# Kernel optimization log

Hardware: AMD Instinct MI355X
Metric: run time of the kernel (lower is better)

Reference implementation:

```python
import jax, jax.numpy as jnp
import numpy as np

N_STATE = 1024
N_HEAD = 16
B = 2
S = 2048


def setup_inputs() -> dict:
    key = jax.random.key(0)
    ks = jax.random.split(key, 8)
    s = 0.02
    x = jax.random.normal(ks[0], (B, S, N_STATE), dtype=jnp.float32)
    # causal additive mask, as in Whisper: upper triangle = -inf
    mask = jnp.where(jnp.triu(jnp.ones((S, S), dtype=bool), k=1), -jnp.inf, 0.0).astype(jnp.float32)
    Wq = jax.random.normal(ks[1], (N_STATE, N_STATE), dtype=jnp.float32) * s
    bq = jax.random.normal(ks[2], (N_STATE,), dtype=jnp.float32) * s
    Wk = jax.random.normal(ks[3], (N_STATE, N_STATE), dtype=jnp.float32) * s
    Wv = jax.random.normal(ks[4], (N_STATE, N_STATE), dtype=jnp.float32) * s
    bv = jax.random.normal(ks[5], (N_STATE,), dtype=jnp.float32) * s
    Wo = jax.random.normal(ks[6], (N_STATE, N_STATE), dtype=jnp.float32) * s
    bo = jax.random.normal(ks[7], (N_STATE,), dtype=jnp.float32) * s
    return {"x": x, "mask": mask, "Wq": Wq, "bq": bq, "Wk": Wk,
            "Wv": Wv, "bv": bv, "Wo": Wo, "bo": bo}


def reference(x, mask, Wq, bq, Wk, Wv, bv, Wo, bo):
    Bb, S_, D = x.shape
    H = N_HEAD
    hd = D // H
    scale = hd ** (-0.25)  # scale split across q and k, as in the source
    q = x @ Wq.T + bq              # [B,S,D]
    k = x @ Wk.T                   # key has no bias
    v = x @ Wv.T + bv
    # [B,S,D] -> [B,H,S,hd]
    q = q.reshape(Bb, S_, H, hd).transpose(0, 2, 1, 3) * scale
    k = k.reshape(Bb, S_, H, hd).transpose(0, 2, 1, 3) * scale
    v = v.reshape(Bb, S_, H, hd).transpose(0, 2, 1, 3)
    qk = jnp.einsum('bhsd,bhtd->bhst', q, k) + mask[:S_, :S_]
    w = jax.nn.softmax(qk, axis=-1).astype(q.dtype)
    out = jnp.einsum('bhst,bhtd->bhsd', w, v)
    out = out.transpose(0, 2, 1, 3).reshape(Bb, S_, D)
    return out @ Wo.T + bo
```

## Files before the change

kernel.cpp:

```cpp
#include <hip/hip_runtime.h>
#include <hip/hip_bf16.h>
#include <cmath>

typedef __bf16 bf16;
typedef __bf16 bf16x8 __attribute__((ext_vector_type(8)));
typedef __bf16 bf16x4 __attribute__((ext_vector_type(4)));
typedef float f32x4 __attribute__((ext_vector_type(4)));

#define QS 0.18033688f

__device__ __forceinline__ void load16_to_lds(const void* g, void* l) {
    __builtin_amdgcn_global_load_lds(
        (const __attribute__((address_space(1))) unsigned int*)g,
        (__attribute__((address_space(3))) unsigned int*)l, 16, 0, 0);
}

__global__ __launch_bounds__(256) void convert_kernel(
    const float* __restrict__ x,  const float* __restrict__ wq,
    const float* __restrict__ wk, const float* __restrict__ wv,
    const float* __restrict__ wo, bf16* __restrict__ dst)
{
    const size_t M1 = 1024ull * 1024ull, M4 = 4ull * M1;
    size_t i0 = ((size_t)blockIdx.x * 256 + threadIdx.x) * 8;
    const float* s;
    size_t off;
    float sc = 1.f;
    if      (i0 < M4)        { s = x;  off = i0; }
    else if (i0 < M4 + M1)   { s = wq; off = i0 - M4; sc = QS; }
    else if (i0 < M4 + 2*M1) { s = wk; off = i0 - M4 - M1; }
    else if (i0 < M4 + 3*M1) { s = wv; off = i0 - M4 - 2*M1; }
    else                     { s = wo; off = i0 - M4 - 3*M1; }
    float4 a = *(const float4*)(s + off);
    float4 b = *(const float4*)(s + off + 4);
    bf16x8 r = { (bf16)(a.x*sc), (bf16)(a.y*sc), (bf16)(a.z*sc), (bf16)(a.w*sc),
                 (bf16)(b.x*sc), (bf16)(b.y*sc), (bf16)(b.z*sc), (bf16)(b.w*sc) };
    *(bf16x8*)(dst + i0) = r;
}

template<int BM, bool OUT_F32>
__device__ __forceinline__ void gemm_core(
    const bf16* __restrict__ A, const bf16* __restrict__ W,
    const float* __restrict__ bias, void* __restrict__ C,
    int mb, int nb, bool vt_out, float bias_scale)
{
    constexpr int IF = BM / 32;
    __shared__ __align__(16) bf16 As[BM * 32];
    __shared__ __align__(16) bf16 Bs[128 * 32];

    const int tid  = threadIdx.x;
    const int lane = tid & 63;
    const int wave = tid >> 6;
    const int wr   = (wave >> 1) * (BM / 2);
    const int wc   = (wave & 1) * 64;
    const int l15  = lane & 15;
    const int l4   = lane >> 4;
    const int swz  = (l4 ^ ((l15 >> 1) & 3)) * 8;

    f32x4 acc[IF][4] = {};

    for (int kt = 0; kt < 32; ++kt) {
#pragma unroll
        for (int it = 0; it < BM / 64; ++it) {
            int c = it * 256 + tid;
            int scol = ((c & 3) ^ ((c >> 3) & 3)) * 8;
            load16_to_lds(&A[(size_t)(mb * BM + (c >> 2)) * 1024 + kt * 32 + scol],
                          &As[(it * 256 + (tid & 192)) * 8]);
        }
#pragma unroll
        for (int it = 0; it < 2; ++it) {
            int c = it * 256 + tid;
            int scol = ((c & 3) ^ ((c >> 3) & 3)) * 8;
            load16_to_lds(&W[(size_t)(nb * 128 + (c >> 2)) * 1024 + kt * 32 + scol],
                          &Bs[(it * 256 + (tid & 192)) * 8]);
        }
        __syncthreads();
        bf16x8 af[IF], bfr[4];
#pragma unroll
        for (int i = 0; i < IF; ++i)
            af[i] = *(const bf16x8*)&As[(wr + i * 16 + l15) * 32 + swz];
#pragma unroll
        for (int j = 0; j < 4; ++j)
            bfr[j] = *(const bf16x8*)&Bs[(wc + j * 16 + l15) * 32 + swz];
#pragma unroll
        for (int i = 0; i < IF; ++i)
#pragma unroll
            for (int j = 0; j < 4; ++j)
                acc[i][j] = __builtin_amdgcn_mfma_f32_16x16x32_bf16(
                    af[i], bfr[j], acc[i][j], 0, 0, 0);
        __syncthreads();
    }

    if (!OUT_F32 && vt_out) {
#pragma unroll
        for (int j = 0; j < 4; ++j) {
            int col = nb * 128 + wc + j * 16 + l15;
            float bv = bias ? bias[col] : 0.f;
            int h = col >> 6, d = col & 63;
#pragma unroll
            for (int i = 0; i < IF; ++i) {
                int m0 = mb * BM + wr + i * 16 + l4 * 4;
                int b = m0 >> 11, s = m0 & 2047;
                bf16x4 pk = { (bf16)(acc[i][j][0] + bv), (bf16)(acc[i][j][1] + bv),
                              (bf16)(acc[i][j][2] + bv), (bf16)(acc[i][j][3] + bv) };
                *(bf16x4*)&((bf16*)C)[(size_t)((b * 16 + h) * 64 + d) * 2048 + s] = pk;
            }
        }
    } else {
#pragma unroll
        for (int j = 0; j < 4; ++j) {
            int col = nb * 128 + wc + j * 16 + l15;
            float bv = bias ? bias[col] * bias_scale : 0.f;
#pragma unroll
            for (int i = 0; i < IF; ++i) {
                int row0 = mb * BM + wr + i * 16 + l4 * 4;
#pragma unroll
                for (int r = 0; r < 4; ++r) {
                    float val = acc[i][j][r] + bv;
                    size_t idx = (size_t)(row0 + r) * 1024 + col;
                    if (OUT_F32) ((float*)C)[idx] = val;
                    else         ((bf16*)C)[idx]  = (bf16)val;
                }
            }
        }
    }
}

__global__ __launch_bounds__(256) void qkv_kernel(
    const bf16* __restrict__ xb,
    const bf16* __restrict__ wqb, const float* __restrict__ bq,
    const bf16* __restrict__ wkb,
    const bf16* __restrict__ wvb, const float* __restrict__ bv,
    bf16* __restrict__ q, bf16* __restrict__ k, bf16* __restrict__ vt)
{
    int mb = blockIdx.x;
    int nbg = blockIdx.y;
    int sel = nbg >> 3, nb = nbg & 7;
    const bf16* W = (sel == 0) ? wqb : ((sel == 1) ? wkb : wvb);
    const float* bias = (sel == 0) ? bq : ((sel == 2) ? bv : nullptr);
    bf16* C = (sel == 0) ? q : ((sel == 1) ? k : vt);
    gemm_core<128, false>(xb, W, bias, C, mb, nb, sel == 2,
                          sel == 0 ? QS : 1.f);
}

__global__ __launch_bounds__(256) void oproj_kernel(
    const bf16* __restrict__ ao, const bf16* __restrict__ wob,
    const float* __restrict__ bo, float* __restrict__ out)
{
    gemm_core<128, true>(ao, wob, bo, out, blockIdx.x, blockIdx.y, false, 1.f);
}

__global__ __launch_bounds__(128) void attn_kernel(
    const bf16* __restrict__ q, const bf16* __restrict__ k,
    const bf16* __restrict__ vt, bf16* __restrict__ o)
{
    __shared__ __align__(16) bf16 Ks[2][64 * 64];
    __shared__ __align__(16) bf16 Vs[2][64 * 64];
    __shared__ __align__(16) bf16 Ps[2][32 * 72];

    const int tid  = threadIdx.x;
    const int lane = tid & 63;
    const int wave = tid >> 6;
    const int l15  = lane & 15;
    const int l4   = lane >> 4;

    const int bh = blockIdx.x;
    const int qt = 31 - blockIdx.y;
    const int b = bh >> 4, h = bh & 15;

    auto stage = [&](int nt, int buf) {
#pragma unroll
        for (int it = 0; it < 4; ++it) {
            int c = it * 128 + tid;
            int scol = ((c & 7) ^ ((c >> 3) & 7)) * 8;
            load16_to_lds(&k[(size_t)(b * 2048 + nt * 64 + (c >> 3)) * 1024 + h * 64 + scol],
                          &Ks[buf][(it * 128 + (tid & 64)) * 8]);
            load16_to_lds(&vt[(size_t)(bh * 64 + (c >> 3)) * 2048 + nt * 64 + scol],
                          &Vs[buf][(it * 128 + (tid & 64)) * 8]);
        }
    };

    int b0 = 0;
    stage(0, 0);

    const int qrow0 = qt * 64 + wave * 32;
    bf16x8 qf[2][2];
#pragma unroll
    for (int qb = 0; qb < 2; ++qb)
#pragma unroll
        for (int kk = 0; kk < 2; ++kk)
            qf[qb][kk] = *(const bf16x8*)&q[(size_t)(b * 2048 + qrow0 + qb * 16 + l15) * 1024
                                           + h * 64 + kk * 32 + l4 * 8];

    f32x4 oacc[2][4] = {};
    float lsum[2] = { 0.f, 0.f };

    const int n = qt + 1;
    for (int nt = 0; nt < n; ++nt) {
        __syncthreads();
        if (nt + 1 < n) stage(nt + 1, b0 ^ 1);

        f32x4 s[2][4] = {};
#pragma unroll
        for (int kk = 0; kk < 2; ++kk) {
#pragma unroll
            for (int j = 0; j < 4; ++j) {
                bf16x8 kf = *(const bf16x8*)&Ks[b0][(j * 16 + l15) * 64
                                + (((kk * 4 + l4) ^ (l15 & 7)) * 8)];
                s[0][j] = __builtin_amdgcn_mfma_f32_16x16x32_bf16(kf, qf[0][kk], s[0][j], 0, 0, 0);
                s[1][j] = __builtin_amdgcn_mfma_f32_16x16x32_bf16(kf, qf[1][kk], s[1][j], 0, 0, 0);
            }
        }

        const bool diag = (nt == qt);
#pragma unroll
        for (int qb = 0; qb < 2; ++qb) {
            float pv[4][4];
            if (diag) {
                int qg = qrow0 + qb * 16 + l15;
#pragma unroll
                for (int j = 0; j < 4; ++j)
#pragma unroll
                    for (int r = 0; r < 4; ++r) {
                        int kg = nt * 64 + j * 16 + l4 * 4 + r;
                        pv[j][r] = (kg > qg) ? 0.f : __builtin_amdgcn_exp2f(s[qb][j][r]);
                    }
            } else {
#pragma unroll
                for (int j = 0; j < 4; ++j)
#pragma unroll
                    for (int r = 0; r < 4; ++r)
                        pv[j][r] = __builtin_amdgcn_exp2f(s[qb][j][r]);
            }
#pragma unroll
            for (int j = 0; j < 4; ++j)
                lsum[qb] += (pv[j][0] + pv[j][1]) + (pv[j][2] + pv[j][3]);

#pragma unroll
            for (int j = 0; j < 4; ++j) {
                bf16x4 pk = { (bf16)pv[j][0], (bf16)pv[j][1], (bf16)pv[j][2], (bf16)pv[j][3] };
                *(bf16x4*)&Ps[wave][(qb * 16 + l15) * 72 + j * 16 + l4 * 4] = pk;
            }
        }

#pragma unroll
        for (int kk = 0; kk < 2; ++kk) {
            bf16x8 pf0 = *(const bf16x8*)&Ps[wave][l15 * 72 + kk * 32 + l4 * 8];
            bf16x8 pf1 = *(const bf16x8*)&Ps[wave][(16 + l15) * 72 + kk * 32 + l4 * 8];
#pragma unroll
            for (int f = 0; f < 4; ++f) {
                bf16x8 vf = *(const bf16x8*)&Vs[b0][(f * 16 + l15) * 64
                                + (((kk * 4 + l4) ^ (l15 & 7)) * 8)];
                oacc[0][f] = __builtin_amdgcn_mfma_f32_16x16x32_bf16(pf0, vf, oacc[0][f], 0, 0, 0);
                oacc[1][f] = __builtin_amdgcn_mfma_f32_16x16x32_bf16(pf1, vf, oacc[1][f], 0, 0, 0);
            }
        }
        b0 ^= 1;
    }

#pragma unroll
    for (int qb = 0; qb < 2; ++qb) {
        float ls = lsum[qb];
        ls += __shfl_xor(ls, 16, 64);
        ls += __shfl_xor(ls, 32, 64);
        float rinv[4];
#pragma unroll
        for (int r = 0; r < 4; ++r) rinv[r] = 1.f / __shfl(ls, l4 * 4 + r, 64);
#pragma unroll
        for (int f = 0; f < 4; ++f)
#pragma unroll
            for (int r = 0; r < 4; ++r)
                o[(size_t)(b * 2048 + qrow0 + qb * 16 + l4 * 4 + r) * 1024 + h * 64 + f * 16 + l15]
                    = (bf16)(oacc[qb][f][r] * rinv[r]);
    }
}

extern "C" void kernel_launch(void* const* d_in, const int* in_sizes, int n_in,
                              void* d_out, int out_size, void* d_ws, size_t ws_size,
                              hipStream_t stream)
{
    const float* x  = (const float*)d_in[0];
    const float* Wq = (const float*)d_in[2];
    const float* bq = (const float*)d_in[3];
    const float* Wk = (const float*)d_in[4];
    const float* Wv = (const float*)d_in[5];
    const float* bv = (const float*)d_in[6];
    const float* Wo = (const float*)d_in[7];
    const float* bo = (const float*)d_in[8];
    float* out = (float*)d_out;

    const size_t M1 = 1024ull * 1024ull, M4 = 4ull * M1;
    bf16* base = (bf16*)d_ws;
    bf16* xb  = base;
    bf16* wqb = base + M4;
    bf16* wkb = base + M4 + M1;
    bf16* wvb = base + M4 + 2 * M1;
    bf16* wob = base + M4 + 3 * M1;
    bf16* q   = base + 8 * M1;
    bf16* k   = base + 12 * M1;
    bf16* vt  = base + 16 * M1;
    bf16* ao  = xb;

    convert_kernel<<<4096, 256, 0, stream>>>(x, Wq, Wk, Wv, Wo, base);
    qkv_kernel<<<dim3(32, 24), 256, 0, stream>>>(xb, wqb, bq, wkb, wvb, bv, q, k, vt);
    attn_kernel<<<dim3(32, 32), 128, 0, stream>>>(q, k, vt, ao);
    oproj_kernel<<<dim3(32, 8), 256, 0, stream>>>(ao, wob, bo, out);
}
```

Before: 193.3 us.

## Write K/V in MFMA fragment order and read them directly from global in attention

The QKV GEMM epilogue now scatters K and V into a per-(batch,head,key-tile) layout that matches the MFMA operand fragments, so each lane reads one contiguous 16-byte chunk. The attention kernel drops its LDS double-buffered K/V staging and syncthreads, instead loading fragments straight from global/L2. It also uses one wave per 32-query block, with a grid twice as large and a launch bound of 4. This removes LDS staging and barriers, but the epilogue now does scalar scattered bf16 stores, and K/V tiles are re-read from cache by more waves.

```diff
diff --git a/kernel.cpp b/kernel.cpp
--- a/kernel.cpp
+++ b/kernel.cpp
@@ -37,11 +37,11 @@
     *(bf16x8*)(dst + i0) = r;
 }
 
-template<int BM, bool OUT_F32>
+template<int BM, int MODE>
 __device__ __forceinline__ void gemm_core(
     const bf16* __restrict__ A, const bf16* __restrict__ W,
     const float* __restrict__ bias, void* __restrict__ C,
-    int mb, int nb, bool vt_out, float bias_scale)
+    int mb, int nb, float bias_scale)
 {
     constexpr int IF = BM / 32;
     __shared__ __align__(16) bf16 As[BM * 32];
@@ -90,19 +90,29 @@
         __syncthreads();
     }
 
-    if (!OUT_F32 && vt_out) {
+    if (MODE == 1 || MODE == 2) {
 #pragma unroll
         for (int j = 0; j < 4; ++j) {
-            int col = nb * 128 + wc + j * 16 + l15;
-            float bv = bias ? bias[col] : 0.f;
-            int h = col >> 6, d = col & 63;
+            int D = nb * 128 + wc + j * 16 + l15;
+            float bv = bias ? bias[D] : 0.f;
+            int hh = D >> 6, d = D & 63;
 #pragma unroll
             for (int i = 0; i < IF; ++i) {
-                int m0 = mb * BM + wr + i * 16 + l4 * 4;
-                int b = m0 >> 11, s = m0 & 2047;
-                bf16x4 pk = { (bf16)(acc[i][j][0] + bv), (bf16)(acc[i][j][1] + bv),
-                              (bf16)(acc[i][j][2] + bv), (bf16)(acc[i][j][3] + bv) };
-                *(bf16x4*)&((bf16*)C)[(size_t)((b * 16 + h) * 64 + d) * 2048 + s] = pk;
+                int S0 = mb * BM + wr + i * 16 + l4 * 4;
+#pragma unroll
+                for (int r = 0; r < 4; ++r) {
+                    int S = S0 + r;
+                    int bb = S >> 11, key = S & 2047;
+                    int bh = bb * 16 + hh, nt = key >> 6, ktl = key & 63;
+                    size_t idx;
+                    if (MODE == 1)
+                        idx = ((size_t)(bh * 32 + nt) * 8 + (d >> 5) * 4 + (ktl >> 4)) * 512
+                            + ((d >> 3) & 3) * 128 + (ktl & 15) * 8 + (d & 7);
+                    else
+                        idx = ((size_t)(bh * 32 + nt) * 8 + (ktl >> 5) * 4 + (d >> 4)) * 512
+                            + ((ktl >> 3) & 3) * 128 + (d & 15) * 8 + (ktl & 7);
+                    ((bf16*)C)[idx] = (bf16)(acc[i][j][r] + bv);
+                }
             }
         }
     } else {
@@ -117,8 +127,8 @@
                 for (int r = 0; r < 4; ++r) {
                     float val = acc[i][j][r] + bv;
                     size_t idx = (size_t)(row0 + r) * 1024 + col;
-                    if (OUT_F32) ((float*)C)[idx] = val;
-                    else         ((bf16*)C)[idx]  = (bf16)val;
+                    if (MODE == 3) ((float*)C)[idx] = val;
+                    else           ((bf16*)C)[idx]  = (bf16)val;
                 }
             }
         }
@@ -130,59 +140,38 @@
     const bf16* __restrict__ wqb, const float* __restrict__ bq,
     const bf16* __restrict__ wkb,
     const bf16* __restrict__ wvb, const float* __restrict__ bv,
-    bf16* __restrict__ q, bf16* __restrict__ k, bf16* __restrict__ vt)
+    bf16* __restrict__ q, bf16* __restrict__ kfb, bf16* __restrict__ vfb)
 {
     int mb = blockIdx.x;
     int nbg = blockIdx.y;
     int sel = nbg >> 3, nb = nbg & 7;
-    const bf16* W = (sel == 0) ? wqb : ((sel == 1) ? wkb : wvb);
-    const float* bias = (sel == 0) ? bq : ((sel == 2) ? bv : nullptr);
-    bf16* C = (sel == 0) ? q : ((sel == 1) ? k : vt);
-    gemm_core<128, false>(xb, W, bias, C, mb, nb, sel == 2,
-                          sel == 0 ? QS : 1.f);
+    if      (sel == 0) gemm_core<128, 0>(xb, wqb, bq,      q,   mb, nb, QS);
+    else if (sel == 1) gemm_core<128, 1>(xb, wkb, nullptr, kfb, mb, nb, 1.f);
+    else               gemm_core<128, 2>(xb, wvb, bv,      vfb, mb, nb, 1.f);
 }
 
 __global__ __launch_bounds__(256) void oproj_kernel(
     const bf16* __restrict__ ao, const bf16* __restrict__ wob,
     const float* __restrict__ bo, float* __restrict__ out)
 {
-    gemm_core<128, true>(ao, wob, bo, out, blockIdx.x, blockIdx.y, false, 1.f);
-}
-
-__global__ __launch_bounds__(128) void attn_kernel(
-    const bf16* __restrict__ q, const bf16* __restrict__ k,
-    const bf16* __restrict__ vt, bf16* __restrict__ o)
-{
-    __shared__ __align__(16) bf16 Ks[2][64 * 64];
-    __shared__ __align__(16) bf16 Vs[2][64 * 64];
-    __shared__ __align__(16) bf16 Ps[2][32 * 72];
-
-    const int tid  = threadIdx.x;
-    const int lane = tid & 63;
-    const int wave = tid >> 6;
+    gemm_core<128, 3>(ao, wob, bo, out, blockIdx.x, blockIdx.y, 1.f);
+}
+
+__global__ __launch_bounds__(64, 4) void attn_kernel(
+    const bf16* __restrict__ q, const bf16* __restrict__ kfb,
+    const bf16* __restrict__ vfb, bf16* __restrict__ o)
+{
+    __shared__ __align__(16) bf16 Ps[32 * 72];
+
+    const int lane = threadIdx.x;
     const int l15  = lane & 15;
     const int l4   = lane >> 4;
 
     const int bh = blockIdx.x;
-    const int qt = 31 - blockIdx.y;
-    const int b = bh >> 4, h = bh & 15;
-
-    auto stage = [&](int nt, int buf) {
-#pragma unroll
-        for (int it = 0; it < 4; ++it) {
-            int c = it * 128 + tid;
-            int scol = ((c & 7) ^ ((c >> 3) & 7)) * 8;
-            load16_to_lds(&k[(size_t)(b * 2048 + nt * 64 + (c >> 3)) * 1024 + h * 64 + scol],
-                          &Ks[buf][(it * 128 + (tid & 64)) * 8]);
-            load16_to_lds(&vt[(size_t)(bh * 64 + (c >> 3)) * 2048 + nt * 64 + scol],
-                          &Vs[buf][(it * 128 + (tid & 64)) * 8]);
-        }
-    };
-
-    int b0 = 0;
-    stage(0, 0);
-
-    const int qrow0 = qt * 64 + wave * 32;
+    const int wt = 63 - blockIdx.y;
+    const int b  = bh >> 4, h = bh & 15;
+    const int qrow0 = wt * 32;
+
     bf16x8 qf[2][2];
 #pragma unroll
     for (int qb = 0; qb < 2; ++qb)
@@ -191,27 +180,29 @@
             qf[qb][kk] = *(const bf16x8*)&q[(size_t)(b * 2048 + qrow0 + qb * 16 + l15) * 1024
                                            + h * 64 + kk * 32 + l4 * 8];
 
+    const bf16* kb = kfb + (size_t)bh * 131072;
+    const bf16* vb = vfb + (size_t)bh * 131072;
+
     f32x4 oacc[2][4] = {};
     float lsum[2] = { 0.f, 0.f };
 
-    const int n = qt + 1;
+    const int n = (qrow0 >> 6) + 1;
     for (int nt = 0; nt < n; ++nt) {
-        __syncthreads();
-        if (nt + 1 < n) stage(nt + 1, b0 ^ 1);
+        const bf16* kt_ = kb + nt * 4096;
+        const bf16* vt_ = vb + nt * 4096;
 
         f32x4 s[2][4] = {};
 #pragma unroll
         for (int kk = 0; kk < 2; ++kk) {
 #pragma unroll
             for (int j = 0; j < 4; ++j) {
-                bf16x8 kf = *(const bf16x8*)&Ks[b0][(j * 16 + l15) * 64
-                                + (((kk * 4 + l4) ^ (l15 & 7)) * 8)];
+                bf16x8 kf = *(const bf16x8*)&kt_[(kk * 4 + j) * 512 + lane * 8];
                 s[0][j] = __builtin_amdgcn_mfma_f32_16x16x32_bf16(kf, qf[0][kk], s[0][j], 0, 0, 0);
                 s[1][j] = __builtin_amdgcn_mfma_f32_16x16x32_bf16(kf, qf[1][kk], s[1][j], 0, 0, 0);
             }
         }
 
-        const bool diag = (nt == qt);
+        const bool diag = (nt == n - 1);
 #pragma unroll
         for (int qb = 0; qb < 2; ++qb) {
             float pv[4][4];
@@ -238,23 +229,21 @@
 #pragma unroll
             for (int j = 0; j < 4; ++j) {
                 bf16x4 pk = { (bf16)pv[j][0], (bf16)pv[j][1], (bf16)pv[j][2], (bf16)pv[j][3] };
-                *(bf16x4*)&Ps[wave][(qb * 16 + l15) * 72 + j * 16 + l4 * 4] = pk;
+                *(bf16x4*)&Ps[(qb * 16 + l15) * 72 + j * 16 + l4 * 4] = pk;
             }
         }
 
 #pragma unroll
         for (int kk = 0; kk < 2; ++kk) {
-            bf16x8 pf0 = *(const bf16x8*)&Ps[wave][l15 * 72 + kk * 32 + l4 * 8];
-            bf16x8 pf1 = *(const bf16x8*)&Ps[wave][(16 + l15) * 72 + kk * 32 + l4 * 8];
+            bf16x8 pf0 = *(const bf16x8*)&Ps[l15 * 72 + kk * 32 + l4 * 8];
+            bf16x8 pf1 = *(const bf16x8*)&Ps[(16 + l15) * 72 + kk * 32 + l4 * 8];
 #pragma unroll
             for (int f = 0; f < 4; ++f) {
-                bf16x8 vf = *(const bf16x8*)&Vs[b0][(f * 16 + l15) * 64
-                                + (((kk * 4 + l4) ^ (l15 & 7)) * 8)];
+                bf16x8 vf = *(const bf16x8*)&vt_[(kk * 4 + f) * 512 + lane * 8];
                 oacc[0][f] = __builtin_amdgcn_mfma_f32_16x16x32_bf16(pf0, vf, oacc[0][f], 0, 0, 0);
                 oacc[1][f] = __builtin_amdgcn_mfma_f32_16x16x32_bf16(pf1, vf, oacc[1][f], 0, 0, 0);
             }
         }
-        b0 ^= 1;
     }
 
 #pragma unroll
@@ -296,12 +285,12 @@
     bf16* wvb = base + M4 + 2 * M1;
     bf16* wob = base + M4 + 3 * M1;
     bf16* q   = base + 8 * M1;
-    bf16* k   = base + 12 * M1;
-    bf16* vt  = base + 16 * M1;
+    bf16* kfb = base + 12 * M1;
+    bf16* vfb = base + 16 * M1;
     bf16* ao  = xb;
 
     convert_kernel<<<4096, 256, 0, stream>>>(x, Wq, Wk, Wv, Wo, base);
-    qkv_kernel<<<dim3(32, 24), 256, 0, stream>>>(xb, wqb, bq, wkb, wvb, bv, q, k, vt);
-    attn_kernel<<<dim3(32, 32), 128, 0, stream>>>(q, k, vt, ao);
+    qkv_kernel<<<dim3(32, 24), 256, 0, stream>>>(xb, wqb, bq, wkb, wvb, bv, q, kfb, vfb);
+    attn_kernel<<<dim3(32, 64), 64, 0, stream>>>(q, kfb, vfb, ao);
     oproj_kernel<<<dim3(32, 8), 256, 0, stream>>>(ao, wob, bo, out);
 }
```

Measured after the change: 195.2 us. About the same (+1.0%).
